# Optimization experiments

Hardware: AMD Instinct MI355X
Metric: run time of the kernel (lower is better)

Reference implementation:

```python
import jax, jax.numpy as jnp
import numpy as np

B, DIM, X, Y = 2, 256, 48, 48
HEADS, DIM_HEAD = 8, 64
DIM_INNER = HEADS * DIM_HEAD
MASK_SELF_VALUE = -100.0
EPS = 1e-12


def setup_inputs() -> dict:
    key = jax.random.key(0)
    k0, k1, k2, k3, k4 = jax.random.split(key, 5)
    return {
        "fmap": jax.random.normal(k0, (B, DIM, X, Y), dtype=jnp.float32),
        "gamma": jnp.ones((DIM,), dtype=jnp.float32),
        "w_qk": jax.random.normal(k1, (DIM_INNER, DIM), dtype=jnp.float32) * 0.02,
        "w_v": jax.random.normal(k2, (DIM_INNER, DIM), dtype=jnp.float32) * 0.02,
        "null_kv": jax.random.normal(k3, (2, HEADS, DIM_HEAD), dtype=jnp.float32),
        "w_out": jax.random.normal(k4, (DIM, DIM_INNER), dtype=jnp.float32) * 0.02,
    }


def _safe_sqrt(d2):
    # matches torch.cdist subgradient: zero grad at zero distance
    pos = d2 > 0
    return jnp.where(pos, jnp.sqrt(jnp.where(pos, d2, 1.0)), 0.0)


def reference(fmap, gamma, w_qk, w_v, null_kv, w_out):
    b, c, x, y = fmap.shape
    h, dh = HEADS, DIM_HEAD
    n = x * y
    scale = dh ** -0.5

    # ChannelRMSNorm: L2-normalize over channel dim, * sqrt(dim) * gamma
    l2 = jnp.sqrt(jnp.sum(fmap * fmap, axis=1, keepdims=True))
    normed = fmap / jnp.maximum(l2, EPS) * jnp.sqrt(jnp.float32(c)) * gamma[None, :, None, None]

    flat = normed.reshape(b, c, n)                       # b c n
    qk = jnp.einsum('oc,bcn->bon', w_qk, flat)           # b (h d) n
    v = jnp.einsum('oc,bcn->bon', w_v, flat)
    qk = qk.reshape(b, h, dh, n).transpose(0, 1, 3, 2)   # b h n d
    v = v.reshape(b, h, dh, n).transpose(0, 1, 3, 2)

    nk = jnp.broadcast_to(null_kv[0][None, :, None, :], (b, h, 1, dh))
    nv = jnp.broadcast_to(null_kv[1][None, :, None, :], (b, h, 1, dh))
    q = qk
    k = jnp.concatenate([nk, qk], axis=2)                # b h (n+1) d
    vv = jnp.concatenate([nv, v], axis=2)

    # -cdist(q, k, p=2) * scale via squared-distance expansion
    q2 = jnp.sum(q * q, axis=-1)[..., :, None]           # b h n 1
    k2 = jnp.sum(k * k, axis=-1)[..., None, :]           # b h 1 n+1
    cross = jnp.einsum('bhid,bhjd->bhij', q, k)          # b h n n+1
    d2 = jnp.maximum(q2 + k2 - 2.0 * cross, 0.0)
    sim = -_safe_sqrt(d2) * scale

    # mask self: eye(n) left-padded by one (null token never masked)
    self_mask = jnp.eye(n, n + 1, k=1, dtype=bool)
    sim = jnp.where(self_mask, MASK_SELF_VALUE, sim)

    attn = jax.nn.softmax(sim, axis=-1)
    out = jnp.einsum('bhij,bhjd->bhid', attn, vv)        # b h n d
    out = out.transpose(0, 1, 3, 2).reshape(b, h * dh, x, y)
    return jnp.einsum('oc,bcxy->boxy', w_out, out)
```

## Files before the change

### kernel.cpp

```cpp
#include <hip/hip_runtime.h>
#include <math.h>

#define NPOS 2304
#define CC   256
#define DI   512
#define NT   36
#define SCALE 0.125f
#define MASKV -100.0f
#define NEGSL2E (-0.18033688011112042f)

typedef __attribute__((ext_vector_type(8))) short bf16x8;
typedef __attribute__((ext_vector_type(4))) float f32x4;
typedef unsigned short u16;
typedef unsigned int u32;

__device__ inline u16 f2bf(float f) {
    union { float f; unsigned int u; } v; v.f = f;
    return (u16)((v.u + 0x7fffu + ((v.u >> 16) & 1u)) >> 16);
}
__device__ inline float bf2f(u16 h) { return __uint_as_float(((u32)h) << 16); }

__device__ inline bf16x8 ld_x8(const u16* p) {
    union { bf16x8 v; uint2 d[2]; } u;
    u.d[0] = *(const uint2*)(p + 0);
    u.d[1] = *(const uint2*)(p + 4);
    return u.v;
}

__device__ __forceinline__ void gl16(const u16* g, u16* l) {
    __builtin_amdgcn_global_load_lds(
        (const __attribute__((address_space(1))) void*)g,
        (__attribute__((address_space(3))) void*)l, 16, 0, 0);
}

__global__ __launch_bounds__(256) void k_proj(const float* __restrict__ fmap,
                                              const float* __restrict__ gamma,
                                              const float* __restrict__ wqk,
                                              const float* __restrict__ wv,
                                              const float* __restrict__ wout,
                                              const float* __restrict__ null_kv,
                                              u16* __restrict__ qkh,
                                              u16* __restrict__ vt,
                                              float* __restrict__ sq,
                                              float* __restrict__ ndot,
                                              float* __restrict__ nk2b,
                                              u16* __restrict__ wo_hi,
                                              u16* __restrict__ wo_lo) {
    const int blk = blockIdx.x;
    if (blk >= 576) {
        const int idx = blk - 576;
#pragma unroll
        for (int it = 0; it < 2; ++it) {
            const int k = idx * 512 + (int)threadIdx.x + it * 256;
            if (k < 32768) {
                const float4 v = ((const float4*)wout)[k];
                ushort4 h4, l4;
                h4.x = f2bf(v.x); l4.x = f2bf(v.x - bf2f(h4.x));
                h4.y = f2bf(v.y); l4.y = f2bf(v.y - bf2f(h4.y));
                h4.z = f2bf(v.z); l4.z = f2bf(v.z - bf2f(h4.z));
                h4.w = f2bf(v.w); l4.w = f2bf(v.w - bf2f(h4.w));
                ((ushort4*)wo_hi)[k] = h4;
                ((ushort4*)wo_lo)[k] = l4;
            }
        }
        return;
    }
    const int xcd = blk & 7;
    const int r   = blk >> 3;
    const int bh  = xcd * 2 + (r & 1);
    const int b   = bh >> 3;
    const int oy  = bh & 7;
    const int n0  = (r >> 1) * 64;

    const int t  = threadIdx.x;
    const int w = t >> 6, lane = t & 63, mcol = lane & 15, quad = lane >> 4;
    const int tx = t & 63, ty = t >> 6;

    __shared__ u16 X[64][260];
    __shared__ float red[4][64];
    __shared__ float inv_s[64];
    __shared__ float gs[256];
    __shared__ float sqp[4][64], ndp[4][64];
    u16 (*Tt)[68] = (u16(*)[68])X;

    gs[t] = gamma[t];
    const float* fb = fmap + (size_t)b * CC * NPOS;
    float v64[64];
#pragma unroll
    for (int i = 0; i < 64; ++i)
        v64[i] = fb[(ty * 64 + i) * NPOS + n0 + tx];
    float s = 0.0f;
#pragma unroll
    for (int i = 0; i < 64; ++i) s += v64[i] * v64[i];
    red[ty][tx] = s;
    __syncthreads();
    if (t < 64) {
        const float tt = red[0][t] + red[1][t] + red[2][t] + red[3][t];
        inv_s[t] = 16.0f / fmaxf(sqrtf(tt), 1e-12f);
    }
    __syncthreads();
    const float iv = inv_s[tx];
#pragma unroll
    for (int i = 0; i < 64; i += 2) {
        const int c = ty * 64 + i;
        const float v0 = v64[i] * iv * gs[c];
        const float v1 = v64[i + 1] * iv * gs[c + 1];
        *(u32*)&X[tx][c] = (u32)f2bf(v0) | ((u32)f2bf(v1) << 16);
    }
    if (blk == 0 && t < 8) {
        float s2 = 0.0f;
#pragma unroll 8
        for (int d = 0; d < 64; ++d) { const float x = null_kv[t * 64 + d]; s2 += x * x; }
        nk2b[t] = s2;
    }
    __syncthreads();

    const size_t wroff = (size_t)(oy * 64 + w * 16 + mcol) * 256 + quad * 8;
    const float* wrq = wqk + wroff;
    const float* wrv = wv + wroff;

    f32x4 cq[4], cv[4];
#pragma unroll
    for (int nf = 0; nf < 4; ++nf) {
        cq[nf] = (f32x4){0.f, 0.f, 0.f, 0.f};
        cv[nf] = (f32x4){0.f, 0.f, 0.f, 0.f};
    }
#pragma unroll
    for (int kc = 0; kc < 8; ++kc) {
        const float4 qa = *(const float4*)&wrq[kc * 32];
        const float4 qb4 = *(const float4*)&wrq[kc * 32 + 4];
        const float4 va = *(const float4*)&wrv[kc * 32];
        const float4 vb4 = *(const float4*)&wrv[kc * 32 + 4];
        bf16x8 aq, av;
        aq[0] = f2bf(qa.x);  aq[1] = f2bf(qa.y);  aq[2] = f2bf(qa.z);  aq[3] = f2bf(qa.w);
        aq[4] = f2bf(qb4.x); aq[5] = f2bf(qb4.y); aq[6] = f2bf(qb4.z); aq[7] = f2bf(qb4.w);
        av[0] = f2bf(va.x);  av[1] = f2bf(va.y);  av[2] = f2bf(va.z);  av[3] = f2bf(va.w);
        av[4] = f2bf(vb4.x); av[5] = f2bf(vb4.y); av[6] = f2bf(vb4.z); av[7] = f2bf(vb4.w);
        bf16x8 xB[4];
#pragma unroll
        for (int nf = 0; nf < 4; ++nf)
            xB[nf] = ld_x8(&X[nf * 16 + mcol][kc * 32 + quad * 8]);
#pragma unroll
        for (int nf = 0; nf < 4; ++nf) {
            cq[nf] = __builtin_amdgcn_mfma_f32_16x16x32_bf16(aq, xB[nf], cq[nf], 0, 0, 0);
            cv[nf] = __builtin_amdgcn_mfma_f32_16x16x32_bf16(av, xB[nf], cv[nf], 0, 0, 0);
        }
    }
    __syncthreads();

    {
        const int h = oy;
        const float4 nk4 = *(const float4*)&null_kv[h * 64 + w * 16 + quad * 4];
        float sv[4], nd[4];
#pragma unroll
        for (int nf = 0; nf < 4; ++nf) {
            sv[nf] = cq[nf][0] * cq[nf][0] + cq[nf][1] * cq[nf][1] + cq[nf][2] * cq[nf][2] + cq[nf][3] * cq[nf][3];
            nd[nf] = cq[nf][0] * nk4.x + cq[nf][1] * nk4.y + cq[nf][2] * nk4.z + cq[nf][3] * nk4.w;
        }
#pragma unroll
        for (int mk = 16; mk <= 32; mk <<= 1)
#pragma unroll
            for (int nf = 0; nf < 4; ++nf) {
                sv[nf] += __shfl_xor(sv[nf], mk);
                nd[nf] += __shfl_xor(nd[nf], mk);
            }
        if (quad == 0) {
#pragma unroll
            for (int nf = 0; nf < 4; ++nf) {
                sqp[w][nf * 16 + mcol] = sv[nf];
                ndp[w][nf * 16 + mcol] = nd[nf];
            }
        }
#pragma unroll
        for (int nf = 0; nf < 4; ++nf) {
            ushort4 r4;
            r4.x = f2bf(cq[nf][0]); r4.y = f2bf(cq[nf][1]);
            r4.z = f2bf(cq[nf][2]); r4.w = f2bf(cq[nf][3]);
            *(ushort4*)&Tt[nf * 16 + mcol][w * 16 + quad * 4] = r4;
        }
        __syncthreads();
        {
            const int n = t >> 2, ds = (t & 3) * 16;
            const uint2 r0 = *(const uint2*)&Tt[n][ds + 0];
            const uint2 r1 = *(const uint2*)&Tt[n][ds + 4];
            const uint2 r2 = *(const uint2*)&Tt[n][ds + 8];
            const uint2 r3 = *(const uint2*)&Tt[n][ds + 12];
            u16* dst = qkh + (((size_t)bh) * NPOS + n0 + n) * 64 + ds;
            *(uint4*)&dst[0] = make_uint4(r0.x, r0.y, r1.x, r1.y);
            *(uint4*)&dst[8] = make_uint4(r2.x, r2.y, r3.x, r3.y);
        }
        if (t < 64) {
            sq  [((size_t)bh) * NPOS + n0 + t] = sqp[0][t] + sqp[1][t] + sqp[2][t] + sqp[3][t];
            ndot[((size_t)bh) * NPOS + n0 + t] = ndp[0][t] + ndp[1][t] + ndp[2][t] + ndp[3][t];
        }
    }
    __syncthreads();

    {
#pragma unroll
        for (int nf = 0; nf < 4; ++nf)
#pragma unroll
            for (int rr = 0; rr < 4; ++rr)
                Tt[w * 16 + quad * 4 + rr][nf * 16 + mcol] = f2bf(cv[nf][rr]);
        __syncthreads();
        {
            const int d = t >> 2, ks = t & 3;
            const uint2 a0 = *(const uint2*)&Tt[d][ks * 16 + 0];
            const uint2 a1 = *(const uint2*)&Tt[d][ks * 16 + 4];
            const uint2 a2 = *(const uint2*)&Tt[d][ks * 16 + 8];
            const uint2 a3 = *(const uint2*)&Tt[d][ks * 16 + 12];
            u16* vdst = vt + (size_t)bh * (72 * 64 * 32);
            const int kb = (n0 >> 5) + (ks >> 1);
            u16* p = &vdst[((size_t)kb * 64 + d) * 32 + (ks & 1) * 16];
            *(uint4*)&p[0] = make_uint4(a0.x, a0.y, a1.x, a1.y);
            *(uint4*)&p[8] = make_uint4(a2.x, a2.y, a3.x, a3.y);
        }
    }
}

__global__ __launch_bounds__(256) void k_attn(const u16* __restrict__ qkh,
                                              const u16* __restrict__ vt,
                                              const float* __restrict__ null_kv,
                                              const float* __restrict__ nk2b,
                                              const float* __restrict__ sq,
                                              const float* __restrict__ ndot,
                                              u16* __restrict__ ih,
                                              u16* __restrict__ il) {
    const int blk = blockIdx.x;
    const int xcd = blk & 7;
    const int j = blk >> 3;
    const int bh = xcd * 2 + (j & 1);
    const int qt = j >> 1;
    const int q0 = qt * 64;
    const int b = bh >> 3, h = bh & 7;
    const int t = threadIdx.x;
    const int wave = t >> 6, lane = t & 63;
    const int mcol = lane & 15, quad = lane >> 4;

    __shared__ __align__(16) u16 sm[20992];
    u16* Kls = sm;
    u16* Vls = sm + 8192;
    u16 (*Pt)[72] = (u16(*)[72])(sm + 16384 + wave * 1152);

    const u16* qbase = qkh + (size_t)bh * NPOS * 64;
    const u16* vbase = vt + (size_t)bh * (72 * 64 * 32);
    const float* sqb = sq + (size_t)bh * NPOS;

    const int q16 = q0 + wave * 16;
    const bf16x8 bq00 = *(const bf16x8*)&qbase[(q16 + mcol) * 64 + quad * 8];
    const bf16x8 bq01 = *(const bf16x8*)&qbase[(q16 + mcol) * 64 + 32 + quad * 8];
    const float q2 = sqb[q16 + mcol];
    const int ktm = q16 >> 6;
    const int nbm = (q16 >> 4) & 3;

    const int kbase0 = (wave * 16 + 0) * 64;
    const int kbase1 = (wave * 16 + 8) * 64;
    const int ksrc0 = (wave * 16 + 0 + (lane >> 3)) * 64 + ((lane & 7) ^ (lane >> 3)) * 8;
    const int ksrc1 = (wave * 16 + 8 + (lane >> 3)) * 64 + ((lane & 7) ^ (lane >> 3)) * 8;
    const int vldsb = wave * 512;
    const int vsrc = (wave * 16 + (lane >> 2)) * 32 + ((lane & 3) ^ ((lane >> 3) & 3)) * 8;

    const int m7 = mcol & 7;
    const int mv = (mcol >> 1) & 3;

    {
        gl16(qbase + ksrc0, Kls + kbase0);
        gl16(qbase + ksrc1, Kls + kbase1);
        gl16(vbase + vsrc,        Vls + vldsb);
        gl16(vbase + 2048 + vsrc, Vls + 2048 + vldsb);
    }

    const bf16x8 ones = {0x3F80, 0x3F80, 0x3F80, 0x3F80, 0x3F80, 0x3F80, 0x3F80, 0x3F80};

    f32x4 oacc[4];
#pragma unroll
    for (int nb = 0; nb < 4; ++nb) oacc[nb] = (f32x4){0.f, 0.f, 0.f, 0.f};
    f32x4 lsum = (f32x4){0.f, 0.f, 0.f, 0.f};

    int p = 0;
#pragma unroll 1
    for (int kt = 0; kt < 36; ++kt) {
        __syncthreads();
        float4 k2q[4];
#pragma unroll
        for (int nb = 0; nb < 4; ++nb)
            k2q[nb] = *(const float4*)&sqb[kt * 64 + nb * 16 + quad * 4];
        if (kt + 1 < 36) {
            const u16* kg = qbase + (size_t)(kt + 1) * 4096;
            const u16* vg = vbase + (size_t)(kt + 1) * 4096;
            const int bb = (p ^ 1) * 4096;
            gl16(kg + ksrc0, Kls + bb + kbase0);
            gl16(kg + ksrc1, Kls + bb + kbase1);
            gl16(vg + vsrc,        Vls + bb + vldsb);
            gl16(vg + 2048 + vsrc, Vls + bb + 2048 + vldsb);
        }

        const u16* Kb = Kls + p * 4096;
        const u16* Vb = Vls + p * 4096;

        bf16x8 bk[4][2];
#pragma unroll
        for (int nb = 0; nb < 4; ++nb) {
            const int rr = (nb * 16 + mcol) * 64;
            bk[nb][0] = *(const bf16x8*)&Kb[rr + ((quad ^ m7)) * 8];
            bk[nb][1] = *(const bf16x8*)&Kb[rr + (((4 + quad) ^ m7)) * 8];
        }

        f32x4 c[4];
#pragma unroll
        for (int nb = 0; nb < 4; ++nb) {
            c[nb] = (f32x4){0.f, 0.f, 0.f, 0.f};
            c[nb] = __builtin_amdgcn_mfma_f32_16x16x32_bf16(bk[nb][0], bq00, c[nb], 0, 0, 0);
            c[nb] = __builtin_amdgcn_mfma_f32_16x16x32_bf16(bk[nb][1], bq01, c[nb], 0, 0, 0);
        }

        bf16x8 bv[4][2];
#pragma unroll
        for (int nb = 0; nb < 4; ++nb) {
            const int rr = (nb * 16 + mcol) * 32 + ((quad ^ mv)) * 8;
            bv[nb][0] = *(const bf16x8*)&Vb[rr];
            bv[nb][1] = *(const bf16x8*)&Vb[2048 + rr];
        }

#pragma unroll
        for (int nb = 0; nb < 4; ++nb) {
            float e[4];
#pragma unroll
            for (int r = 0; r < 4; ++r) {
                const float pre = q2 + ((const float*)&k2q[nb])[r];
                const float d2 = fmaxf(__builtin_fmaf(c[nb][r], -2.0f, pre), 0.0f);
                e[r] = __builtin_amdgcn_exp2f(NEGSL2E * __builtin_amdgcn_sqrtf(d2));
            }
            if (kt == ktm && nb == nbm) {
#pragma unroll
                for (int r = 0; r < 4; ++r)
                    if (quad * 4 + r == mcol) e[r] = 0.0f;
            }
            const u32 p01 = __builtin_amdgcn_perm(__float_as_uint(e[1]), __float_as_uint(e[0]), 0x07060302u);
            const u32 p23 = __builtin_amdgcn_perm(__float_as_uint(e[3]), __float_as_uint(e[2]), 0x07060302u);
            *(uint2*)&Pt[mcol][nb * 16 + quad * 4] = make_uint2(p01, p23);
        }

        const bf16x8 bp00 = *(const bf16x8*)&Pt[mcol][quad * 8];
        const bf16x8 bp01 = *(const bf16x8*)&Pt[mcol][32 + quad * 8];

#pragma unroll
        for (int nb = 0; nb < 4; ++nb) {
            oacc[nb] = __builtin_amdgcn_mfma_f32_16x16x32_bf16(bv[nb][0], bp00, oacc[nb], 0, 0, 0);
            oacc[nb] = __builtin_amdgcn_mfma_f32_16x16x32_bf16(bv[nb][1], bp01, oacc[nb], 0, 0, 0);
        }
        lsum = __builtin_amdgcn_mfma_f32_16x16x32_bf16(ones, bp00, lsum, 0, 0, 0);
        lsum = __builtin_amdgcn_mfma_f32_16x16x32_bf16(ones, bp01, lsum, 0, 0, 0);

        p ^= 1;
    }

    __syncthreads();

    float* Ofin = (float*)sm + wave * (16 * 68);
#pragma unroll
    for (int nb = 0; nb < 4; ++nb)
        *(f32x4*)&Ofin[mcol * 68 + nb * 16 + quad * 4] = oacc[nb];
    if (quad == 0) Ofin[mcol * 68 + 64] = lsum[0];

    {
        const int q = lane >> 2;
        const int d0 = (lane & 3) * 16;
        const float4 a0 = *(const float4*)&Ofin[q * 68 + d0 + 0];
        const float4 a1 = *(const float4*)&Ofin[q * 68 + d0 + 4];
        const float4 a2 = *(const float4*)&Ofin[q * 68 + d0 + 8];
        const float4 a3 = *(const float4*)&Ofin[q * 68 + d0 + 12];
        const float l = Ofin[q * 68 + 64];

        const int qg = q16 + q;
        const float q2v = sqb[qg];
        const float nd = ndot[(size_t)bh * NPOS + qg];
        const float nk2 = nk2b[h];
        const float d2n = fmaxf(q2v + nk2 - 2.0f * nd, 0.0f);
        const float beta = __expf(-sqrtf(d2n) * SCALE);
        const float ilv = 1.0f / (l + beta);

        const float* nvp = &null_kv[DI + h * 64 + d0];
        const float4 nv0 = *(const float4*)&nvp[0];
        const float4 nv1 = *(const float4*)&nvp[4];
        const float4 nv2 = *(const float4*)&nvp[8];
        const float4 nv3 = *(const float4*)&nvp[12];

        const size_t ob = ((size_t)b * NPOS + qg) * DI + h * 64 + d0;
        float vv[16];
        vv[0]  = (a0.x + beta * nv0.x) * ilv; vv[1]  = (a0.y + beta * nv0.y) * ilv;
        vv[2]  = (a0.z + beta * nv0.z) * ilv; vv[3]  = (a0.w + beta * nv0.w) * ilv;
        vv[4]  = (a1.x + beta * nv1.x) * ilv; vv[5]  = (a1.y + beta * nv1.y) * ilv;
        vv[6]  = (a1.z + beta * nv1.z) * ilv; vv[7]  = (a1.w + beta * nv1.w) * ilv;
        vv[8]  = (a2.x + beta * nv2.x) * ilv; vv[9]  = (a2.y + beta * nv2.y) * ilv;
        vv[10] = (a2.z + beta * nv2.z) * ilv; vv[11] = (a2.w + beta * nv2.w) * ilv;
        vv[12] = (a3.x + beta * nv3.x) * ilv; vv[13] = (a3.y + beta * nv3.y) * ilv;
        vv[14] = (a3.z + beta * nv3.z) * ilv; vv[15] = (a3.w + beta * nv3.w) * ilv;
#pragma unroll
        for (int g = 0; g < 4; ++g) {
            ushort4 hi4, lo4;
            hi4.x = f2bf(vv[g * 4 + 0]); lo4.x = f2bf(vv[g * 4 + 0] - bf2f(hi4.x));
            hi4.y = f2bf(vv[g * 4 + 1]); lo4.y = f2bf(vv[g * 4 + 1] - bf2f(hi4.y));
            hi4.z = f2bf(vv[g * 4 + 2]); lo4.z = f2bf(vv[g * 4 + 2] - bf2f(hi4.z));
            hi4.w = f2bf(vv[g * 4 + 3]); lo4.w = f2bf(vv[g * 4 + 3] - bf2f(hi4.w));
            *(ushort4*)&ih[ob + g * 4] = hi4;
            *(ushort4*)&il[ob + g * 4] = lo4;
        }
    }
}

__global__ __launch_bounds__(256) void k_out(const u16* __restrict__ wo_hi,
                                             const u16* __restrict__ wo_lo,
                                             const u16* __restrict__ ih,
                                             const u16* __restrict__ il,
                                             float* __restrict__ out) {
    const int j0 = blockIdx.x * 32;
    const int c0 = blockIdx.y * 64;
    const int b  = blockIdx.z;
    const int t  = threadIdx.x;
    const int w = t >> 6, lane = t & 63, mcol = lane & 15, quad = lane >> 4;

    const u16* ah = wo_hi + (size_t)(c0 + w * 16 + mcol) * 512 + quad * 8;
    const u16* al = wo_lo + (size_t)(c0 + w * 16 + mcol) * 512 + quad * 8;
    const u16* xh = ih + ((size_t)b * NPOS + j0 + mcol) * 512 + quad * 8;
    const u16* xl = il + ((size_t)b * NPOS + j0 + mcol) * 512 + quad * 8;

    f32x4 c[2];
#pragma unroll
    for (int nf = 0; nf < 2; ++nf) c[nf] = (f32x4){0.f, 0.f, 0.f, 0.f};
#pragma unroll
    for (int kc = 0; kc < 16; ++kc) {
        const bf16x8 A  = *(const bf16x8*)&ah[kc * 32];
        const bf16x8 Al = *(const bf16x8*)&al[kc * 32];
        bf16x8 Bh[2], Bl[2];
#pragma unroll
        for (int nf = 0; nf < 2; ++nf) {
            Bh[nf] = *(const bf16x8*)&xh[(size_t)nf * 16 * 512 + kc * 32];
            Bl[nf] = *(const bf16x8*)&xl[(size_t)nf * 16 * 512 + kc * 32];
        }
#pragma unroll
        for (int nf = 0; nf < 2; ++nf) {
            c[nf] = __builtin_amdgcn_mfma_f32_16x16x32_bf16(A,  Bh[nf], c[nf], 0, 0, 0);
            c[nf] = __builtin_amdgcn_mfma_f32_16x16x32_bf16(A,  Bl[nf], c[nf], 0, 0, 0);
            c[nf] = __builtin_amdgcn_mfma_f32_16x16x32_bf16(Al, Bh[nf], c[nf], 0, 0, 0);
        }
    }
    float* ob = out + ((size_t)b * CC + c0 + w * 16) * NPOS + j0;
#pragma unroll
    for (int nf = 0; nf < 2; ++nf)
#pragma unroll
        for (int r = 0; r < 4; ++r)
            ob[(size_t)(quad * 4 + r) * NPOS + nf * 16 + mcol] = c[nf][r];
}

extern "C" void kernel_launch(void* const* d_in, const int* in_sizes, int n_in,
                              void* d_out, int out_size, void* d_ws, size_t ws_size,
                              hipStream_t stream) {
    const float* fmap    = (const float*)d_in[0];
    const float* gamma   = (const float*)d_in[1];
    const float* w_qk    = (const float*)d_in[2];
    const float* w_v     = (const float*)d_in[3];
    const float* null_kv = (const float*)d_in[4];
    const float* w_out   = (const float*)d_in[5];
    float* out = (float*)d_out;

    u16* ws16 = (u16*)d_ws;
    u16* qkh    = ws16;
    u16* vtb    = qkh + 2359296;
    u16* in_hi  = vtb + 2359296;
    u16* in_lo  = in_hi + 2359296;
    u16* wo_hi  = in_lo + 2359296;
    u16* wo_lo  = wo_hi + 131072;
    float* sqbuf = (float*)(wo_lo + 131072);
    float* ndbuf = sqbuf + 36864;
    float* nk2b  = ndbuf + 36864;

    hipLaunchKernelGGL(k_proj, dim3(648),       dim3(256), 0, stream,
                       fmap, gamma, w_qk, w_v, w_out, null_kv, qkh, vtb, sqbuf, ndbuf, nk2b, wo_hi, wo_lo);
    hipLaunchKernelGGL(k_attn, dim3(576),       dim3(256), 0, stream,
                       qkh, vtb, null_kv, nk2b, sqbuf, ndbuf, in_hi, in_lo);
    hipLaunchKernelGGL(k_out,  dim3(72, 4, 2),  dim3(256), 0, stream,
                       wo_hi, wo_lo, in_hi, in_lo, out);
}
```

Measured before the change: 179.2 us.

## Split attention key range in two with a separate merge kernel

The attention kernel gains a template mode that processes half of the key tiles per block, doubling the grid from 576 to 1152 blocks. Unnormalized partial outputs and row sums go to fp32 workspace buffers. A new merge kernel adds the two halves, applies the null-key term and normalization, then writes the hi/lo bf16 split. The aim is better CU fill and less tail imbalance, paid for with an extra launch and roughly 19 MB of extra fp32 write/read traffic. The split path is taken only when the workspace is large enough; otherwise the original single-pass kernel runs.

```diff
diff --git a/kernel.cpp b/kernel.cpp
--- a/kernel.cpp
+++ b/kernel.cpp
@@ -218,6 +218,7 @@
     }
 }
 
+template <int KS>
 __global__ __launch_bounds__(256) void k_attn(const u16* __restrict__ qkh,
                                               const u16* __restrict__ vt,
                                               const float* __restrict__ null_kv,
@@ -225,17 +226,24 @@
                                               const float* __restrict__ sq,
                                               const float* __restrict__ ndot,
                                               u16* __restrict__ ih,
-                                              u16* __restrict__ il) {
+                                              u16* __restrict__ il,
+                                              float* __restrict__ pO,
+                                              float* __restrict__ pL) {
     const int blk = blockIdx.x;
     const int xcd = blk & 7;
     const int j = blk >> 3;
     const int bh = xcd * 2 + (j & 1);
-    const int qt = j >> 1;
+    const int r2 = j >> 1;
+    const int qt = (KS == 2) ? (r2 >> 1) : r2;
+    const int kh = (KS == 2) ? (r2 & 1) : 0;
     const int q0 = qt * 64;
     const int b = bh >> 3, h = bh & 7;
     const int t = threadIdx.x;
     const int wave = t >> 6, lane = t & 63;
     const int mcol = lane & 15, quad = lane >> 4;
+
+    const int kt0 = kh * 18;
+    const int NTL = (KS == 2) ? 18 : 36;
 
     __shared__ __align__(16) u16 sm[20992];
     u16* Kls = sm;
@@ -264,10 +272,12 @@
     const int mv = (mcol >> 1) & 3;
 
     {
-        gl16(qbase + ksrc0, Kls + kbase0);
-        gl16(qbase + ksrc1, Kls + kbase1);
-        gl16(vbase + vsrc,        Vls + vldsb);
-        gl16(vbase + 2048 + vsrc, Vls + 2048 + vldsb);
+        const u16* kg = qbase + (size_t)kt0 * 4096;
+        const u16* vg = vbase + (size_t)kt0 * 4096;
+        gl16(kg + ksrc0, Kls + kbase0);
+        gl16(kg + ksrc1, Kls + kbase1);
+        gl16(vg + vsrc,        Vls + vldsb);
+        gl16(vg + 2048 + vsrc, Vls + 2048 + vldsb);
     }
 
     const bf16x8 ones = {0x3F80, 0x3F80, 0x3F80, 0x3F80, 0x3F80, 0x3F80, 0x3F80, 0x3F80};
@@ -279,13 +289,14 @@
 
     int p = 0;
 #pragma unroll 1
-    for (int kt = 0; kt < 36; ++kt) {
+    for (int i = 0; i < NTL; ++i) {
+        const int kt = kt0 + i;
         __syncthreads();
         float4 k2q[4];
 #pragma unroll
         for (int nb = 0; nb < 4; ++nb)
             k2q[nb] = *(const float4*)&sqb[kt * 64 + nb * 16 + quad * 4];
-        if (kt + 1 < 36) {
+        if (i + 1 < NTL) {
             const u16* kg = qbase + (size_t)(kt + 1) * 4096;
             const u16* vg = vbase + (size_t)(kt + 1) * 4096;
             const int bb = (p ^ 1) * 4096;
@@ -371,41 +382,114 @@
         const float4 a2 = *(const float4*)&Ofin[q * 68 + d0 + 8];
         const float4 a3 = *(const float4*)&Ofin[q * 68 + d0 + 12];
         const float l = Ofin[q * 68 + 64];
-
         const int qg = q16 + q;
-        const float q2v = sqb[qg];
-        const float nd = ndot[(size_t)bh * NPOS + qg];
-        const float nk2 = nk2b[h];
-        const float d2n = fmaxf(q2v + nk2 - 2.0f * nd, 0.0f);
-        const float beta = __expf(-sqrtf(d2n) * SCALE);
-        const float ilv = 1.0f / (l + beta);
-
-        const float* nvp = &null_kv[DI + h * 64 + d0];
-        const float4 nv0 = *(const float4*)&nvp[0];
-        const float4 nv1 = *(const float4*)&nvp[4];
-        const float4 nv2 = *(const float4*)&nvp[8];
-        const float4 nv3 = *(const float4*)&nvp[12];
-
-        const size_t ob = ((size_t)b * NPOS + qg) * DI + h * 64 + d0;
-        float vv[16];
-        vv[0]  = (a0.x + beta * nv0.x) * ilv; vv[1]  = (a0.y + beta * nv0.y) * ilv;
-        vv[2]  = (a0.z + beta * nv0.z) * ilv; vv[3]  = (a0.w + beta * nv0.w) * ilv;
-        vv[4]  = (a1.x + beta * nv1.x) * ilv; vv[5]  = (a1.y + beta * nv1.y) * ilv;
-        vv[6]  = (a1.z + beta * nv1.z) * ilv; vv[7]  = (a1.w + beta * nv1.w) * ilv;
-        vv[8]  = (a2.x + beta * nv2.x) * ilv; vv[9]  = (a2.y + beta * nv2.y) * ilv;
-        vv[10] = (a2.z + beta * nv2.z) * ilv; vv[11] = (a2.w + beta * nv2.w) * ilv;
-        vv[12] = (a3.x + beta * nv3.x) * ilv; vv[13] = (a3.y + beta * nv3.y) * ilv;
-        vv[14] = (a3.z + beta * nv3.z) * ilv; vv[15] = (a3.w + beta * nv3.w) * ilv;
-#pragma unroll
-        for (int g = 0; g < 4; ++g) {
-            ushort4 hi4, lo4;
-            hi4.x = f2bf(vv[g * 4 + 0]); lo4.x = f2bf(vv[g * 4 + 0] - bf2f(hi4.x));
-            hi4.y = f2bf(vv[g * 4 + 1]); lo4.y = f2bf(vv[g * 4 + 1] - bf2f(hi4.y));
-            hi4.z = f2bf(vv[g * 4 + 2]); lo4.z = f2bf(vv[g * 4 + 2] - bf2f(hi4.z));
-            hi4.w = f2bf(vv[g * 4 + 3]); lo4.w = f2bf(vv[g * 4 + 3] - bf2f(hi4.w));
-            *(ushort4*)&ih[ob + g * 4] = hi4;
-            *(ushort4*)&il[ob + g * 4] = lo4;
-        }
+
+        if (KS == 2) {
+            float* dst = pO + (size_t)kh * 2359296 + ((size_t)bh * NPOS + qg) * 64 + d0;
+            *(float4*)&dst[0]  = a0;
+            *(float4*)&dst[4]  = a1;
+            *(float4*)&dst[8]  = a2;
+            *(float4*)&dst[12] = a3;
+            if ((lane & 3) == 0)
+                pL[(size_t)kh * 36864 + (size_t)bh * NPOS + qg] = l;
+        } else {
+            const float q2v = sqb[qg];
+            const float nd = ndot[(size_t)bh * NPOS + qg];
+            const float nk2 = nk2b[h];
+            const float d2n = fmaxf(q2v + nk2 - 2.0f * nd, 0.0f);
+            const float beta = __expf(-sqrtf(d2n) * SCALE);
+            const float ilv = 1.0f / (l + beta);
+
+            const float* nvp = &null_kv[DI + h * 64 + d0];
+            const float4 nv0 = *(const float4*)&nvp[0];
+            const float4 nv1 = *(const float4*)&nvp[4];
+            const float4 nv2 = *(const float4*)&nvp[8];
+            const float4 nv3 = *(const float4*)&nvp[12];
+
+            const size_t ob = ((size_t)b * NPOS + qg) * DI + h * 64 + d0;
+            float vv[16];
+            vv[0]  = (a0.x + beta * nv0.x) * ilv; vv[1]  = (a0.y + beta * nv0.y) * ilv;
+            vv[2]  = (a0.z + beta * nv0.z) * ilv; vv[3]  = (a0.w + beta * nv0.w) * ilv;
+            vv[4]  = (a1.x + beta * nv1.x) * ilv; vv[5]  = (a1.y + beta * nv1.y) * ilv;
+            vv[6]  = (a1.z + beta * nv1.z) * ilv; vv[7]  = (a1.w + beta * nv1.w) * ilv;
+            vv[8]  = (a2.x + beta * nv2.x) * ilv; vv[9]  = (a2.y + beta * nv2.y) * ilv;
+            vv[10] = (a2.z + beta * nv2.z) * ilv; vv[11] = (a2.w + beta * nv2.w) * ilv;
+            vv[12] = (a3.x + beta * nv3.x) * ilv; vv[13] = (a3.y + beta * nv3.y) * ilv;
+            vv[14] = (a3.z + beta * nv3.z) * ilv; vv[15] = (a3.w + beta * nv3.w) * ilv;
+#pragma unroll
+            for (int g = 0; g < 4; ++g) {
+                ushort4 hi4, lo4;
+                hi4.x = f2bf(vv[g * 4 + 0]); lo4.x = f2bf(vv[g * 4 + 0] - bf2f(hi4.x));
+                hi4.y = f2bf(vv[g * 4 + 1]); lo4.y = f2bf(vv[g * 4 + 1] - bf2f(hi4.y));
+                hi4.z = f2bf(vv[g * 4 + 2]); lo4.z = f2bf(vv[g * 4 + 2] - bf2f(hi4.z));
+                hi4.w = f2bf(vv[g * 4 + 3]); lo4.w = f2bf(vv[g * 4 + 3] - bf2f(hi4.w));
+                *(ushort4*)&ih[ob + g * 4] = hi4;
+                *(ushort4*)&il[ob + g * 4] = lo4;
+            }
+        }
+    }
+}
+
+__global__ __launch_bounds__(256) void k_merge(const float* __restrict__ pO,
+                                               const float* __restrict__ pL,
+                                               const float* __restrict__ null_kv,
+                                               const float* __restrict__ nk2b,
+                                               const float* __restrict__ sq,
+                                               const float* __restrict__ ndot,
+                                               u16* __restrict__ ih,
+                                               u16* __restrict__ il) {
+    const int gid = blockIdx.x * 256 + (int)threadIdx.x;
+    const int d0 = (gid & 3) * 16;
+    const int t2 = gid >> 2;
+    const int bh = t2 / NPOS;
+    const int qg = t2 - bh * NPOS;
+    const int b = bh >> 3, h = bh & 7;
+
+    const size_t o0 = ((size_t)bh * NPOS + qg) * 64 + d0;
+    const size_t o1 = o0 + 2359296;
+    const float4 a0 = *(const float4*)&pO[o0 + 0];
+    const float4 a1 = *(const float4*)&pO[o0 + 4];
+    const float4 a2 = *(const float4*)&pO[o0 + 8];
+    const float4 a3 = *(const float4*)&pO[o0 + 12];
+    const float4 c0 = *(const float4*)&pO[o1 + 0];
+    const float4 c1 = *(const float4*)&pO[o1 + 4];
+    const float4 c2 = *(const float4*)&pO[o1 + 8];
+    const float4 c3 = *(const float4*)&pO[o1 + 12];
+    const float l = pL[(size_t)bh * NPOS + qg] + pL[36864 + (size_t)bh * NPOS + qg];
+
+    const float q2v = sq[(size_t)bh * NPOS + qg];
+    const float nd = ndot[(size_t)bh * NPOS + qg];
+    const float nk2 = nk2b[h];
+    const float d2n = fmaxf(q2v + nk2 - 2.0f * nd, 0.0f);
+    const float beta = __expf(-sqrtf(d2n) * SCALE);
+    const float ilv = 1.0f / (l + beta);
+
+    const float* nvp = &null_kv[DI + h * 64 + d0];
+    const float4 nv0 = *(const float4*)&nvp[0];
+    const float4 nv1 = *(const float4*)&nvp[4];
+    const float4 nv2 = *(const float4*)&nvp[8];
+    const float4 nv3 = *(const float4*)&nvp[12];
+
+    float vv[16];
+    vv[0]  = (a0.x + c0.x + beta * nv0.x) * ilv; vv[1]  = (a0.y + c0.y + beta * nv0.y) * ilv;
+    vv[2]  = (a0.z + c0.z + beta * nv0.z) * ilv; vv[3]  = (a0.w + c0.w + beta * nv0.w) * ilv;
+    vv[4]  = (a1.x + c1.x + beta * nv1.x) * ilv; vv[5]  = (a1.y + c1.y + beta * nv1.y) * ilv;
+    vv[6]  = (a1.z + c1.z + beta * nv1.z) * ilv; vv[7]  = (a1.w + c1.w + beta * nv1.w) * ilv;
+    vv[8]  = (a2.x + c2.x + beta * nv2.x) * ilv; vv[9]  = (a2.y + c2.y + beta * nv2.y) * ilv;
+    vv[10] = (a2.z + c2.z + beta * nv2.z) * ilv; vv[11] = (a2.w + c2.w + beta * nv2.w) * ilv;
+    vv[12] = (a3.x + c3.x + beta * nv3.x) * ilv; vv[13] = (a3.y + c3.y + beta * nv3.y) * ilv;
+    vv[14] = (a3.z + c3.z + beta * nv3.z) * ilv; vv[15] = (a3.w + c3.w + beta * nv3.w) * ilv;
+
+    const size_t ob = ((size_t)b * NPOS + qg) * DI + h * 64 + d0;
+#pragma unroll
+    for (int g = 0; g < 4; ++g) {
+        ushort4 hi4, lo4;
+        hi4.x = f2bf(vv[g * 4 + 0]); lo4.x = f2bf(vv[g * 4 + 0] - bf2f(hi4.x));
+        hi4.y = f2bf(vv[g * 4 + 1]); lo4.y = f2bf(vv[g * 4 + 1] - bf2f(hi4.y));
+        hi4.z = f2bf(vv[g * 4 + 2]); lo4.z = f2bf(vv[g * 4 + 2] - bf2f(hi4.z));
+        hi4.w = f2bf(vv[g * 4 + 3]); lo4.w = f2bf(vv[g * 4 + 3] - bf2f(hi4.w));
+        *(ushort4*)&ih[ob + g * 4] = hi4;
+        *(ushort4*)&il[ob + g * 4] = lo4;
     }
 }
 
@@ -474,11 +558,21 @@
     float* sqbuf = (float*)(wo_lo + 131072);
     float* ndbuf = sqbuf + 36864;
     float* nk2b  = ndbuf + 36864;
+    float* pOws  = nk2b + 8;
+    float* pLws  = pOws + 4718592;
+    const size_t need_split = (size_t)((char*)(pLws + 73728) - (char*)d_ws);
 
     hipLaunchKernelGGL(k_proj, dim3(648),       dim3(256), 0, stream,
                        fmap, gamma, w_qk, w_v, w_out, null_kv, qkh, vtb, sqbuf, ndbuf, nk2b, wo_hi, wo_lo);
-    hipLaunchKernelGGL(k_attn, dim3(576),       dim3(256), 0, stream,
-                       qkh, vtb, null_kv, nk2b, sqbuf, ndbuf, in_hi, in_lo);
+    if (ws_size >= need_split) {
+        hipLaunchKernelGGL(HIP_KERNEL_NAME(k_attn<2>), dim3(1152), dim3(256), 0, stream,
+                           qkh, vtb, null_kv, nk2b, sqbuf, ndbuf, in_hi, in_lo, pOws, pLws);
+        hipLaunchKernelGGL(k_merge, dim3(576),  dim3(256), 0, stream,
+                           pOws, pLws, null_kv, nk2b, sqbuf, ndbuf, in_hi, in_lo);
+    } else {
+        hipLaunchKernelGGL(HIP_KERNEL_NAME(k_attn<1>), dim3(576), dim3(256), 0, stream,
+                           qkh, vtb, null_kv, nk2b, sqbuf, ndbuf, in_hi, in_lo, pOws, pLws);
+    }
     hipLaunchKernelGGL(k_out,  dim3(72, 4, 2),  dim3(256), 0, stream,
                        wo_hi, wo_lo, in_hi, in_lo, out);
 }
```

After: 178.6 us. About the same (-0.4%).
